# Performance work log

Hardware: AMD Instinct MI355X
Metric: run time of the kernel (lower is better)

The kernel has to match this reference:

```python
import jax, jax.numpy as jnp
import numpy as np

B, T, C = 4, 2048, 768
H, D = 12, 64          # num_heads, head_size
R = 64                 # kv_lora_rank
ROPE_THETA = 10000.0


def setup_inputs() -> dict:
    key = jax.random.key(0)
    ks = jax.random.split(key, 8)
    s = lambda fan_in: 1.0 / np.sqrt(fan_in)
    return {
        "x":      jax.random.normal(ks[0], (B, T, C), jnp.float32),
        "Wq":     jax.random.normal(ks[1], (C, H * D), jnp.float32) * s(C),
        "Wdown":  jax.random.normal(ks[2], (C, R), jnp.float32) * s(C),
        "ln_g":   jnp.ones((R,), jnp.float32),
        "ln_b":   jnp.zeros((R,), jnp.float32),
        "Wup":    jax.random.normal(ks[3], (R, 2 * H * D), jnp.float32) * s(R),
        "Wo":     jax.random.normal(ks[4], (H * D, C), jnp.float32) * s(H * D),
        "bo":     jnp.zeros((C,), jnp.float32),
    }


def _rope_cos_sin(t, d, dtype):
    # freqs over half-dim, repeated twice (rotate-half convention)
    inv_freq = 1.0 / (ROPE_THETA ** (jnp.arange(0, d, 2, dtype=jnp.float32) / d))
    ang = jnp.arange(t, dtype=jnp.float32)[:, None] * inv_freq[None, :]  # [T, D/2]
    ang = jnp.concatenate([ang, ang], axis=-1)                            # [T, D]
    return jnp.cos(ang).astype(dtype), jnp.sin(ang).astype(dtype)


def _apply_rope(q, cos, sin):
    # q: [B, H, T, D]; cos/sin: [T, D]
    d2 = q.shape[-1] // 2
    rot = jnp.concatenate([-q[..., d2:], q[..., :d2]], axis=-1)
    return q * cos + rot * sin


def reference(x, Wq, Wdown, ln_g, ln_b, Wup, Wo, bo):
    b, t, c = x.shape
    q = (x @ Wq).reshape(b, t, H, D).transpose(0, 2, 1, 3)  # [B,H,T,D]

    ckv = x @ Wdown                                         # [B,T,R]
    mu = jnp.mean(ckv, axis=-1, keepdims=True)
    var = jnp.var(ckv, axis=-1, keepdims=True)
    ckv = (ckv - mu) * jax.lax.rsqrt(var + 1e-5) * ln_g + ln_b

    kv = (ckv @ Wup).reshape(b, t, 2, H, D)
    k = kv[:, :, 0].transpose(0, 2, 1, 3)                   # [B,H,T,D]
    v = kv[:, :, 1].transpose(0, 2, 1, 3)

    cos, sin = _rope_cos_sin(t, D, x.dtype)
    q = _apply_rope(q, cos, sin)
    k = _apply_rope(k, cos, sin)

    wei = jnp.einsum("bhqd,bhkd->bhqk", q, k) * (D ** -0.5)
    causal = jnp.tril(jnp.ones((t, t), bool))
    wei = jnp.where(causal, wei, -jnp.inf)
    wei = jax.nn.softmax(wei, axis=-1)                      # dropout: eval mode (identity)

    out = jnp.einsum("bhqk,bhkd->bhqd", wei, v)             # [B,H,T,D]
    out = out.transpose(0, 2, 1, 3).reshape(b, t, H * D)
    return out @ Wo + bo
```

## Files before the change

kernel.cpp:

```cpp
#include <hip/hip_runtime.h>
#include <hip/hip_bf16.h>
#include <math.h>

#define B_ 4
#define T_ 2048
#define C_ 768
#define H_ 12
#define D_ 64
#define R_ 64
#define BT_ (B_*T_)
#define HD_ (H_*D_)

typedef __attribute__((ext_vector_type(8))) short bf16x8;
typedef __attribute__((ext_vector_type(4))) float f32x4;

__device__ inline short f2bf(float f) {
  union { float f; unsigned u; } x; x.f = f;
  unsigned r = x.u + 0x7fffu + ((x.u >> 16) & 1u);
  return (short)(r >> 16);
}
__device__ inline float bf2f(short s) {
  union { unsigned u; float f; } x; x.u = ((unsigned)(unsigned short)s) << 16;
  return x.f;
}
__device__ inline unsigned pk_bf16(float a, float b) {
#if __has_builtin(__builtin_amdgcn_cvt_pk_bf16_f32)
  auto t = __builtin_amdgcn_cvt_pk_bf16_f32(a, b);
  unsigned u; __builtin_memcpy(&u, &t, sizeof(unsigned)); return u;
#else
  union { float f; unsigned u; } x, y; x.f = a; y.f = b;
  unsigned ra = (x.u + 0x7fffu + ((x.u >> 16) & 1u)) >> 16;
  unsigned rb = (y.u + 0x7fffu + ((y.u >> 16) & 1u)) & 0xffff0000u;
  return ra | rb;
#endif
}
__device__ inline float fexp2(float x) {
#if __has_builtin(__builtin_amdgcn_exp2f)
  return __builtin_amdgcn_exp2f(x);
#else
  return exp2f(x);
#endif
}
typedef __attribute__((address_space(3))) unsigned lds_u32;
typedef __attribute__((address_space(1))) const unsigned glb_u32;
__device__ inline void gload_lds16(const void* g, void* l) {
  __builtin_amdgcn_global_load_lds((glb_u32*)g, (lds_u32*)l, 16, 0, 0);
}

__global__ void convert_f32_bf16(const float* __restrict__ in, short* __restrict__ out, int n4) {
  int i = blockIdx.x * blockDim.x + threadIdx.x;
  if (i < n4) {
    float4 v = ((const float4*)in)[i];
    short4 o;
    o.x = f2bf(v.x); o.y = f2bf(v.y); o.z = f2bf(v.z); o.w = f2bf(v.w);
    ((short4*)out)[i] = o;
  }
}

__device__ inline void ttile(const float* __restrict__ src, short* __restrict__ dst,
                             int K, int N, int k0, int n0, int tid, float (*tl)[33]) {
  int tx = tid & 31, ty = tid >> 5;
  #pragma unroll
  for (int r = 0; r < 4; ++r)
    tl[ty + 8 * r][tx] = src[(size_t)(k0 + ty + 8 * r) * N + n0 + tx];
  __syncthreads();
  #pragma unroll
  for (int r = 0; r < 4; ++r)
    dst[(size_t)(n0 + ty + 8 * r) * K + k0 + tx] = f2bf(tl[tx][ty + 8 * r]);
}

__global__ __launch_bounds__(256) void prep_all(
    const float* __restrict__ Wq, const float* __restrict__ Wd,
    const float* __restrict__ Wup, const float* __restrict__ Wo,
    short* __restrict__ W1T, short* __restrict__ WupT, short* __restrict__ WoT,
    float* __restrict__ cs, float* __restrict__ sn) {
  __shared__ float tl[32][33];
  int blk = blockIdx.x, tid = threadIdx.x;
  if (blk < 576) {
    int tk = blk % 24, tn = blk / 24;
    ttile(Wq, W1T, 768, 768, tk * 32, tn * 32, tid, tl);
  } else if (blk < 624) {
    int l = blk - 576; int tk = l % 24, tn = l / 24;
    ttile(Wd, W1T + (size_t)768 * 768, 768, 64, tk * 32, tn * 32, tid, tl);
  } else if (blk < 720) {
    int l = blk - 624; int tk = l % 2, tn = l / 2;
    ttile(Wup, WupT, 64, 1536, tk * 32, tn * 32, tid, tl);
  } else if (blk < 1296) {
    int l = blk - 720; int tk = l % 24, tn = l / 24;
    ttile(Wo, WoT, 768, 768, tk * 32, tn * 32, tid, tl);
  } else {
    int base = (blk - 1296) * 1024;
    #pragma unroll
    for (int i = 0; i < 4; ++i) {
      int idx = base + tid + i * 256;
      int j = idx & 31, t = idx >> 5;
      float invf = exp2f(-(float)j * (13.287712379549449f / 32.f));
      float a = (float)t * invf;
      cs[idx] = cosf(a);
      sn[idx] = sinf(a);
    }
  }
}

#define SC2_ 0.18033688f

template<int MODE>
__global__ __launch_bounds__(256) void gemm128(
    const short* __restrict__ A, const short* __restrict__ Bt,
    int M, int N, int K, int NBvalid,
    float* __restrict__ out0, const float* __restrict__ bias,
    const float* __restrict__ bias2,
    short* __restrict__ ob0, short* __restrict__ ob1,
    const float* __restrict__ cs, const float* __restrict__ sn)
{
  __shared__ short As[128 * 64];
  __shared__ short Bs[128 * 64];
  const int m0 = blockIdx.x * 128;
  const int n0 = blockIdx.y * 128;
  const int tid = threadIdx.x, lane = tid & 63, w = tid >> 6;
  const int wr = w >> 1, wc = w & 1;
  const int fr = lane & 15, fk = (lane >> 4) * 8;
  const int rstage = lane >> 3;
  const int cstage = (lane & 7) * 8;

  f32x4 acc[4][4] = {};

  for (int k0 = 0; k0 < K; k0 += 64) {
    __syncthreads();
    #pragma unroll
    for (int i = 0; i < 4; ++i) {
      int c = w * 4 + i;
      int r = c * 8 + rstage;
      gload_lds16(&A[(size_t)(m0 + r) * K + k0 + cstage], &As[c * 512]);
      if (n0 + c * 8 < NBvalid)
        gload_lds16(&Bt[(size_t)(n0 + r) * K + k0 + cstage], &Bs[c * 512]);
    }
    __syncthreads();
    #pragma unroll
    for (int kk = 0; kk < 64; kk += 32) {
      bf16x8 a[4], b[4];
      #pragma unroll
      for (int i = 0; i < 4; ++i) {
        a[i] = *(const bf16x8*)&As[(wr * 64 + i * 16 + fr) * 64 + kk + fk];
        b[i] = *(const bf16x8*)&Bs[(wc * 64 + i * 16 + fr) * 64 + kk + fk];
      }
      #pragma unroll
      for (int mi = 0; mi < 4; ++mi)
        #pragma unroll
        for (int ni = 0; ni < 4; ++ni)
          acc[mi][ni] = __builtin_amdgcn_mfma_f32_16x16x32_bf16(a[mi], b[ni], acc[mi][ni], 0, 0, 0);
    }
  }

  const int er = (lane >> 4) * 4, ec = lane & 15;
  const int colbase = n0 + wc * 64;

  if constexpr (MODE == 2) {
    #pragma unroll
    for (int mi = 0; mi < 4; ++mi)
      #pragma unroll
      for (int r = 0; r < 4; ++r) {
        int row = m0 + wr * 64 + mi * 16 + er + r;
        #pragma unroll
        for (int ni = 0; ni < 4; ++ni) {
          int col = colbase + ni * 16 + ec;
          out0[(size_t)row * N + col] = acc[mi][ni][r] + bias[col];
        }
      }
    return;
  }

  if constexpr (MODE == 0) {
    if (colbase < 768) {
      int h = colbase >> 6;
      #pragma unroll
      for (int mi = 0; mi < 4; ++mi)
        #pragma unroll
        for (int r = 0; r < 4; ++r) {
          int row = m0 + wr * 64 + mi * 16 + er + r;
          int t = row & (T_ - 1), bb = row >> 11;
          short* dst = ob0 + (((size_t)(bb * H_ + h)) * T_ + t) * 64;
          #pragma unroll
          for (int ni = 0; ni < 2; ++ni) {
            int d = ni * 16 + ec;
            float c = cs[t * 32 + d] * SC2_, s = sn[t * 32 + d] * SC2_;
            float x0 = acc[mi][ni][r], x1 = acc[mi][ni + 2][r];
            dst[d]      = f2bf(x0 * c - x1 * s);
            dst[d + 32] = f2bf(x1 * c + x0 * s);
          }
        }
    } else if (colbase < 832) {
      #pragma unroll
      for (int mi = 0; mi < 4; ++mi)
        #pragma unroll
        for (int r = 0; r < 4; ++r) {
          float s = 0.f, s2 = 0.f;
          #pragma unroll
          for (int ni = 0; ni < 4; ++ni) { float v = acc[mi][ni][r]; s += v; s2 += v*v; }
          #pragma unroll
          for (int off = 1; off < 16; off <<= 1) {
            s  += __shfl_xor(s, off);
            s2 += __shfl_xor(s2, off);
          }
          float mu = s * (1.f/64.f);
          float var = s2 * (1.f/64.f) - mu * mu;
          float rstd = rsqrtf(var + 1e-5f);
          int row = m0 + wr * 64 + mi * 16 + er + r;
          #pragma unroll
          for (int ni = 0; ni < 4; ++ni) {
            int d = ni * 16 + ec;
            ob1[(size_t)row * 64 + d] = f2bf((acc[mi][ni][r] - mu) * rstd * bias[d] + bias2[d]);
          }
        }
    }
  } else {
    if (colbase < 768) {
      int h = colbase >> 6;
      #pragma unroll
      for (int mi = 0; mi < 4; ++mi)
        #pragma unroll
        for (int r = 0; r < 4; ++r) {
          int row = m0 + wr * 64 + mi * 16 + er + r;
          int t = row & (T_ - 1), bb = row >> 11;
          short* dst = ob0 + (((size_t)(bb * H_ + h)) * T_ + t) * 64;
          #pragma unroll
          for (int ni = 0; ni < 2; ++ni) {
            int d = ni * 16 + ec;
            float c = cs[t * 32 + d], s = sn[t * 32 + d];
            float x0 = acc[mi][ni][r], x1 = acc[mi][ni + 2][r];
            dst[d]      = f2bf(x0 * c - x1 * s);
            dst[d + 32] = f2bf(x1 * c + x0 * s);
          }
        }
    } else {
      __syncthreads();
      short* Wl = (w < 2) ? &As[w * 4096] : &Bs[(w - 2) * 4096];
      int h = (colbase - 768) >> 6;
      #pragma unroll
      for (int mi = 0; mi < 4; ++mi) {
        int tl0 = mi * 16 + er;
        #pragma unroll
        for (int ni = 0; ni < 4; ++ni) {
          int d = ni * 16 + ec;
          int col = (tl0 + (d & 7) * 8) & 63;
          uint2 uu;
          uu.x = pk_bf16(acc[mi][ni][0], acc[mi][ni][1]);
          uu.y = pk_bf16(acc[mi][ni][2], acc[mi][ni][3]);
          *(uint2*)&Wl[d * 64 + col] = uu;
        }
      }
      __syncthreads();
      int bb = m0 >> 11;
      int tg0 = (m0 & (T_ - 1)) + wr * 64;
      int dlow = lane >> 3, tc = lane & 7;
      #pragma unroll
      for (int j = 0; j < 8; ++j) {
        int d = j * 8 + dlow;
        int col = (tc * 8 + (d & 7) * 8) & 63;
        uint4 vv = *(const uint4*)&Wl[d * 64 + col];
        *(uint4*)&ob1[((size_t)(bb * H_ + h) * 64 + d) * T_ + tg0 + tc * 8] = vv;
      }
    }
  }
}

__global__ __launch_bounds__(256) void attn_mfma(
    const short* __restrict__ qgl, const short* __restrict__ kg,
    const short* __restrict__ vtg, short* __restrict__ o)
{
  __shared__ short Ks[2][4096];
  __shared__ short Vts[2][4096];
  __shared__ short Ps[4 * 16 * 72];

  const int bh = blockIdx.x;
  const int y  = blockIdx.y;
  const int qt1 = 31 - y, qt2 = y;
  const int tid = threadIdx.x, lane = tid & 63, w = tid >> 6;
  const int q16 = lane & 15, quad = lane >> 4;
  short* Pw = &Ps[w * 16 * 72];
  const short* kb  = kg  + (size_t)bh * T_ * 64;
  const short* vtb = vtg + (size_t)bh * 64 * T_;
  const int b = bh / H_, h = bh - b * H_;

  const int qbase[2] = {qt1 * 64 + w * 16, qt2 * 64 + w * 16};
  bf16x8 bq[2][2];
  #pragma unroll
  for (int g = 0; g < 2; ++g) {
    const short* qrow = qgl + ((size_t)bh * T_ + qbase[g] + q16) * 64;
    bq[g][0] = *(const bf16x8*)&qrow[quad * 8];
    bq[g][1] = *(const bf16x8*)&qrow[32 + quad * 8];
  }

  f32x4 oacc[2][4] = {};
  float lrun[2] = {0.f, 0.f};
  const int last  = qt1 * 64;
  const int last2 = qt2 * 64;

  auto stage = [&](int kt, int ib) {
    #pragma unroll
    for (int i = 0; i < 2; ++i) {
      int c = w * 2 + i;
      int s = c >> 1, ch = c & 1;
      gload_lds16(kb  + (size_t)(kt + s * 16 + q16) * 64 + ch * 32 + quad * 8, &Ks[ib][c * 512]);
      gload_lds16(vtb + (size_t)(s * 16 + q16) * T_ + kt + ch * 32 + quad * 8, &Vts[ib][c * 512]);
    }
  };

  stage(0, 0);
  int ib = 0;
  for (int kt = 0; kt <= last; kt += 64, ib ^= 1) {
    __syncthreads();
    if (kt + 64 <= last) stage(kt + 64, ib ^ 1);

    #pragma unroll
    for (int g = 0; g < 2; ++g) {
      if (g == 1 && kt > last2) break;
      const int diag_end = (g == 0) ? last : last2;
      const int qidx = qbase[g] + q16;

      f32x4 sacc[4];
      #pragma unroll
      for (int s = 0; s < 4; ++s) {
        bf16x8 a0 = *(const bf16x8*)&Ks[ib][(s * 2 + 0) * 512 + lane * 8];
        bf16x8 a1 = *(const bf16x8*)&Ks[ib][(s * 2 + 1) * 512 + lane * 8];
        f32x4 t0 = {};
        t0 = __builtin_amdgcn_mfma_f32_16x16x32_bf16(a0, bq[g][0], t0, 0, 0, 0);
        t0 = __builtin_amdgcn_mfma_f32_16x16x32_bf16(a1, bq[g][1], t0, 0, 0, 0);
        sacc[s] = t0;
      }

      float pv[16];
      float ls = 0.f;
      if (kt != diag_end) {
        #pragma unroll
        for (int s = 0; s < 4; ++s)
          #pragma unroll
          for (int r = 0; r < 4; ++r) {
            float p = fexp2(sacc[s][r]);
            pv[s * 4 + r] = p; ls += p;
          }
      } else {
        #pragma unroll
        for (int s = 0; s < 4; ++s)
          #pragma unroll
          for (int r = 0; r < 4; ++r) {
            int key = kt + s * 16 + quad * 4 + r;
            float p = (key <= qidx) ? fexp2(sacc[s][r]) : 0.f;
            pv[s * 4 + r] = p; ls += p;
          }
      }
      ls += __shfl_xor(ls, 16);
      ls += __shfl_xor(ls, 32);
      lrun[g] += ls;

      #pragma unroll
      for (int s = 0; s < 4; ++s) {
        uint2 uu;
        uu.x = pk_bf16(pv[s * 4 + 0], pv[s * 4 + 1]);
        uu.y = pk_bf16(pv[s * 4 + 2], pv[s * 4 + 3]);
        *(uint2*)&Pw[q16 * 72 + s * 16 + quad * 4] = uu;
      }

      #pragma unroll
      for (int c = 0; c < 2; ++c) {
        bf16x8 bp = *(const bf16x8*)&Pw[q16 * 72 + c * 32 + quad * 8];
        #pragma unroll
        for (int ms = 0; ms < 4; ++ms) {
          bf16x8 av = *(const bf16x8*)&Vts[ib][(ms * 2 + c) * 512 + lane * 8];
          oacc[g][ms] = __builtin_amdgcn_mfma_f32_16x16x32_bf16(av, bp, oacc[g][ms], 0, 0, 0);
        }
      }
    }
  }

  #pragma unroll
  for (int g = 0; g < 2; ++g) {
    float inv = 1.f / lrun[g];
    #pragma unroll
    for (int ms = 0; ms < 4; ++ms) {
      uint2 uu;
      uu.x = pk_bf16(oacc[g][ms][0] * inv, oacc[g][ms][1] * inv);
      uu.y = pk_bf16(oacc[g][ms][2] * inv, oacc[g][ms][3] * inv);
      *(uint2*)&Pw[q16 * 72 + ms * 16 + quad * 4] = uu;
    }
    int row = lane >> 2, cc2 = (lane & 3) * 16;
    uint4 r0 = *(const uint4*)&Pw[row * 72 + cc2];
    uint4 r1 = *(const uint4*)&Pw[row * 72 + cc2 + 8];
    int t = qbase[g] + row;
    short* orow = o + ((size_t)(b * T_ + t)) * HD_ + h * 64 + cc2;
    *(uint4*)&orow[0] = r0;
    *(uint4*)&orow[8] = r1;
  }
}

extern "C" void kernel_launch(void* const* d_in, const int* in_sizes, int n_in,
                              void* d_out, int out_size, void* d_ws, size_t ws_size,
                              hipStream_t stream) {
  (void)in_sizes; (void)n_in; (void)out_size; (void)ws_size;
  const float* x     = (const float*)d_in[0];
  const float* Wq    = (const float*)d_in[1];
  const float* Wdown = (const float*)d_in[2];
  const float* ln_g  = (const float*)d_in[3];
  const float* ln_b  = (const float*)d_in[4];
  const float* Wup   = (const float*)d_in[5];
  const float* Wo    = (const float*)d_in[6];
  const float* bo    = (const float*)d_in[7];
  float* out = (float*)d_out;

  char* w = (char*)d_ws;
  short* x_bf   = (short*)w;  w += (size_t)BT_ * C_    * 2;
  short* W1T    = (short*)w;  w += (size_t)832 * C_    * 2;
  short* WupT   = (short*)w;  w += (size_t)2*HD_ * R_  * 2;
  short* WoT    = (short*)w;  w += (size_t)HD_ * C_    * 2;
  short* ckv    = (short*)w;  w += (size_t)BT_ * R_    * 2;
  short* qb     = (short*)w;  w += (size_t)BT_ * HD_   * 2;
  short* kb     = (short*)w;  w += (size_t)BT_ * HD_   * 2;
  short* vt     = (short*)w;  w += (size_t)BT_ * HD_   * 2;
  short* att    = (short*)w;  w += (size_t)BT_ * HD_   * 2;
  float* cs_t   = (float*)w;  w += (size_t)T_ * 32 * 4;
  float* sn_t   = (float*)w;  w += (size_t)T_ * 32 * 4;

  prep_all<<<1360, 256, 0, stream>>>(Wq, Wdown, Wup, Wo, W1T, WupT, WoT, cs_t, sn_t);
  convert_f32_bf16<<<(BT_*C_/4 + 255)/256, 256, 0, stream>>>(x, x_bf, BT_*C_/4);

  gemm128<0><<<dim3(BT_/128, 7), 256, 0, stream>>>(
      x_bf, W1T, BT_, 896, C_, 832, nullptr, ln_g, ln_b, qb, ckv, cs_t, sn_t);

  gemm128<1><<<dim3(BT_/128, 12), 256, 0, stream>>>(
      ckv, WupT, BT_, 2*HD_, R_, 2*HD_, nullptr, nullptr, nullptr, kb, vt, cs_t, sn_t);

  attn_mfma<<<dim3(B_*H_, 16), 256, 0, stream>>>(qb, kb, vt, att);

  gemm128<2><<<dim3(BT_/128, 6), 256, 0, stream>>>(
      att, WoT, BT_, C_, HD_, C_, out, bo, nullptr, nullptr, nullptr, nullptr, nullptr);
}
```

Measured before the change: 222.8 us.

## Load K and V tiles directly into registers instead of double-buffered LDS

```diff
diff --git a/kernel.cpp b/kernel.cpp
--- a/kernel.cpp
+++ b/kernel.cpp
@@ -268,16 +268,13 @@
     const short* __restrict__ qgl, const short* __restrict__ kg,
     const short* __restrict__ vtg, short* __restrict__ o)
 {
-  __shared__ short Ks[2][4096];
-  __shared__ short Vts[2][4096];
-  __shared__ short Ps[4 * 16 * 72];
+  __shared__ short Ps[8][1168];
 
   const int bh = blockIdx.x;
   const int y  = blockIdx.y;
   const int qt1 = 31 - y, qt2 = y;
   const int tid = threadIdx.x, lane = tid & 63, w = tid >> 6;
   const int q16 = lane & 15, quad = lane >> 4;
-  short* Pw = &Ps[w * 16 * 72];
   const short* kb  = kg  + (size_t)bh * T_ * 64;
   const short* vtb = vtg + (size_t)bh * 64 * T_;
   const int b = bh / H_, h = bh - b * H_;
@@ -296,36 +293,36 @@
   const int last  = qt1 * 64;
   const int last2 = qt2 * 64;
 
-  auto stage = [&](int kt, int ib) {
-    #pragma unroll
-    for (int i = 0; i < 2; ++i) {
-      int c = w * 2 + i;
-      int s = c >> 1, ch = c & 1;
-      gload_lds16(kb  + (size_t)(kt + s * 16 + q16) * 64 + ch * 32 + quad * 8, &Ks[ib][c * 512]);
-      gload_lds16(vtb + (size_t)(s * 16 + q16) * T_ + kt + ch * 32 + quad * 8, &Vts[ib][c * 512]);
-    }
-  };
-
-  stage(0, 0);
-  int ib = 0;
-  for (int kt = 0; kt <= last; kt += 64, ib ^= 1) {
-    __syncthreads();
-    if (kt + 64 <= last) stage(kt + 64, ib ^ 1);
+  const short* krow = kb + (size_t)q16 * 64 + quad * 8;
+  const short* vrow = vtb + (size_t)q16 * T_ + quad * 8;
+
+  for (int kt = 0; kt <= last; kt += 64) {
+    bf16x8 ak[4][2];
+    #pragma unroll
+    for (int s = 0; s < 4; ++s)
+      #pragma unroll
+      for (int hh = 0; hh < 2; ++hh)
+        ak[s][hh] = *(const bf16x8*)&krow[(size_t)(kt + s * 16) * 64 + hh * 32];
+    bf16x8 av[2][4];
+    #pragma unroll
+    for (int c = 0; c < 2; ++c)
+      #pragma unroll
+      for (int ms = 0; ms < 4; ++ms)
+        av[c][ms] = *(const bf16x8*)&vrow[(size_t)(ms * 16) * T_ + kt + c * 32];
 
     #pragma unroll
     for (int g = 0; g < 2; ++g) {
       if (g == 1 && kt > last2) break;
       const int diag_end = (g == 0) ? last : last2;
       const int qidx = qbase[g] + q16;
+      short* Pw = Ps[w * 2 + g];
 
       f32x4 sacc[4];
       #pragma unroll
       for (int s = 0; s < 4; ++s) {
-        bf16x8 a0 = *(const bf16x8*)&Ks[ib][(s * 2 + 0) * 512 + lane * 8];
-        bf16x8 a1 = *(const bf16x8*)&Ks[ib][(s * 2 + 1) * 512 + lane * 8];
         f32x4 t0 = {};
-        t0 = __builtin_amdgcn_mfma_f32_16x16x32_bf16(a0, bq[g][0], t0, 0, 0, 0);
-        t0 = __builtin_amdgcn_mfma_f32_16x16x32_bf16(a1, bq[g][1], t0, 0, 0, 0);
+        t0 = __builtin_amdgcn_mfma_f32_16x16x32_bf16(ak[s][0], bq[g][0], t0, 0, 0, 0);
+        t0 = __builtin_amdgcn_mfma_f32_16x16x32_bf16(ak[s][1], bq[g][1], t0, 0, 0, 0);
         sacc[s] = t0;
       }
 
@@ -365,10 +362,8 @@
       for (int c = 0; c < 2; ++c) {
         bf16x8 bp = *(const bf16x8*)&Pw[q16 * 72 + c * 32 + quad * 8];
         #pragma unroll
-        for (int ms = 0; ms < 4; ++ms) {
-          bf16x8 av = *(const bf16x8*)&Vts[ib][(ms * 2 + c) * 512 + lane * 8];
-          oacc[g][ms] = __builtin_amdgcn_mfma_f32_16x16x32_bf16(av, bp, oacc[g][ms], 0, 0, 0);
-        }
+        for (int ms = 0; ms < 4; ++ms)
+          oacc[g][ms] = __builtin_amdgcn_mfma_f32_16x16x32_bf16(av[c][ms], bp, oacc[g][ms], 0, 0, 0);
       }
     }
   }
@@ -376,6 +371,7 @@
   #pragma unroll
   for (int g = 0; g < 2; ++g) {
     float inv = 1.f / lrun[g];
+    short* Pw = Ps[w * 2 + g];
     #pragma unroll
     for (int ms = 0; ms < 4; ++ms) {
       uint2 uu;
```

Result: slower. 309.2 us (+38.8%).
